# Optimization experiments

Hardware: AMD Instinct MI355X
Metric: run time of the kernel (lower is better)

Reference implementation:

```python
import jax, jax.numpy as jnp
import numpy as np

D_MODEL = 1024
N_HEADS = 16
HEAD_DIM = D_MODEL // N_HEADS


def setup_inputs() -> dict:
    key = jax.random.key(0)
    k1, k2, k3, k4, k5 = jax.random.split(key, 5)
    s = 0.02
    return {
        "x": jax.random.normal(k1, (2, 2048, D_MODEL), dtype=jnp.float32),
        "w_qkv": jax.random.normal(k2, (D_MODEL, 3 * D_MODEL), dtype=jnp.float32) * s,
        "b_qkv": jax.random.normal(k3, (3 * D_MODEL,), dtype=jnp.float32) * s,
        "w_proj": jax.random.normal(k4, (D_MODEL, D_MODEL), dtype=jnp.float32) * s,
        "b_proj": jax.random.normal(k5, (D_MODEL,), dtype=jnp.float32) * s,
    }


def reference(x, w_qkv, b_qkv, w_proj, b_proj):
    B, T, C = x.shape
    # fused qkv projection: [B,T,3C] -> [3,B,H,T,Dh]
    qkv = x @ w_qkv + b_qkv
    qkv = qkv.reshape(B, T, 3, N_HEADS, HEAD_DIM).transpose(2, 0, 3, 1, 4)
    q, k, v = qkv[0], qkv[1], qkv[2]
    scale = 1.0 / np.sqrt(HEAD_DIM).astype(np.float32)
    att = jnp.einsum("bhtd,bhsd->bhts", q, k) * scale  # [B,H,T,T]
    causal = jnp.triu(jnp.ones((T, T), dtype=bool), k=1)
    att = jnp.where(causal, -jnp.inf, att)
    att = jax.nn.softmax(att, axis=-1)
    # dropout is identity in eval / p=0
    out = jnp.einsum("bhts,bhsd->bhtd", att, v)  # [B,H,T,Dh]
    out = out.transpose(0, 2, 1, 3).reshape(B, T, C)
    return out @ w_proj + b_proj
```

## Files before the change

### kernel.cpp

```cpp
#include <hip/hip_runtime.h>
#include <hip/hip_bf16.h>
#include <stdint.h>

#define MROWS 4096
#define DMODEL 1024
#define NQKV 3072
#define TSEQ 2048

typedef __attribute__((ext_vector_type(8))) short short8;
typedef __attribute__((ext_vector_type(4))) short short4v;
typedef __attribute__((ext_vector_type(4))) float floatx4;
typedef unsigned short ushort_t;

#define TILE_ELEMS 4608
#define BH_TILE_STRIDE 147456

#define QSCALE 0.1803368801111204f

static __device__ __forceinline__ unsigned short f2bf(float f) {
    union { float f; unsigned u; } v; v.f = f;
    unsigned r = v.u + 0x7fff + ((v.u >> 16) & 1);
    return (unsigned short)(r >> 16);
}


static __device__ __forceinline__ floatx4 mfma16(short4v a, short4v b, floatx4 c) {
#if defined(__HIP_DEVICE_COMPILE__)
#if __has_builtin(__builtin_amdgcn_mfma_f32_16x16x16bf16_1k)
    return __builtin_amdgcn_mfma_f32_16x16x16bf16_1k(a, b, c, 0, 0, 0);
#else
#error "mfma 16x16x16 bf16 builtin unavailable on device"
#endif
#else
    return c;
#endif
}

static __device__ __forceinline__ unsigned pk2bf(float a, float b) {
    unsigned ua = __float_as_uint(a) + 0x8000u;
    unsigned ub = __float_as_uint(b) + 0x8000u;
#if defined(__HIP_DEVICE_COMPILE__) && __has_builtin(__builtin_amdgcn_perm)
    return __builtin_amdgcn_perm(ub, ua, 0x07060302u);
#else
    return (ua >> 16) | (ub & 0xFFFF0000u);
#endif
}

static __device__ __forceinline__ float exp2_fast(float x) {
#if defined(__HIP_DEVICE_COMPILE__) && __has_builtin(__builtin_amdgcn_exp2f)
    return __builtin_amdgcn_exp2f(x);
#else
    return exp2f(x);
#endif
}

static __device__ __forceinline__ void glds16(const void* g, void* l) {
    __builtin_amdgcn_global_load_lds(
        (const __attribute__((address_space(1))) void*)g,
        (__attribute__((address_space(3))) void*)l, 16, 0, 0);
}

__global__ void cast_f32_bf16(const float* __restrict__ in,
                              ushort_t* __restrict__ out, int n) {
    int i = (blockIdx.x * blockDim.x + threadIdx.x) * 4;
    if (i < n) {
        float4 f = *(const float4*)(in + i);
        ushort4 o;
        o.x = f2bf(f.x); o.y = f2bf(f.y); o.z = f2bf(f.z); o.w = f2bf(f.w);
        *(ushort4*)(out + i) = o;
    }
}

__global__ void transpose_cast(const float* __restrict__ in,
                               ushort_t* __restrict__ out, int R, int C) {
    __shared__ float tile[32][33];
    int c0 = blockIdx.x * 32, r0 = blockIdx.y * 32;
    int tx = threadIdx.x & 31, ty = threadIdx.x >> 5;
    for (int i = 0; i < 4; i++) {
        int r = ty + i * 8;
        tile[r][tx] = in[(size_t)(r0 + r) * C + c0 + tx];
    }
    __syncthreads();
    for (int i = 0; i < 4; i++) {
        int r = ty + i * 8;
        out[(size_t)(c0 + r) * R + r0 + tx] = f2bf(tile[tx][r]);
    }
}

__global__ void transpose_v(const ushort_t* __restrict__ in,
                            ushort_t* __restrict__ out) {
    __shared__ ushort_t T[64][72];
    int tile = blockIdx.x, bh = blockIdx.y;
    int tid = threadIdx.x;
    int row = tid >> 2, q4 = tid & 3;
    const ushort_t* ip = in + ((size_t)bh * TSEQ + tile * 64) * 64;
#pragma unroll
    for (int p = 0; p < 2; p++) {
        int c = q4 * 16 + p * 8;
        *(uint4*)(&T[row][c]) = *(const uint4*)(ip + (size_t)row * 64 + c);
    }
    __syncthreads();
    ushort_t* op = out + (size_t)bh * BH_TILE_STRIDE + (size_t)tile * TILE_ELEMS;
#pragma unroll
    for (int p = 0; p < 2; p++) {
        int cbase = q4 * 16 + p * 8;
        ushort_t tmp[8];
#pragma unroll
        for (int e = 0; e < 8; e++) {
            int cp = cbase + e;
            int Q = cp >> 4, SB = (cp >> 2) & 3, J = cp & 3;
            int s = SB * 16 + Q * 4 + J;
            tmp[e] = T[s][row];
        }
        *(uint4*)(op + (size_t)row * 72 + cbase) = *(uint4*)tmp;
    }
}

template <int EPI, int MFRAG, int PERXCD>
__global__ __launch_bounds__(256, 3)
void gemm_glds(const ushort_t* __restrict__ A,
               const ushort_t* __restrict__ Bt,
               const float* __restrict__ bias,
               void* __restrict__ out0, void* __restrict__ out1, void* __restrict__ out2,
               int M, int N, int K) {
    __shared__ ushort_t As[MFRAG * 32 * 32];
    __shared__ ushort_t Bs[128 * 32];
    int tid = threadIdx.x;
    int wave = tid >> 6, lane = tid & 63;
    int quad = lane >> 4, l16 = lane & 15;
    int id = blockIdx.x;
    int xcd = id & 7, sidx = id >> 3;
    int m_idx = xcd * PERXCD + (sidx & (PERXCD - 1));
    int n_idx = sidx / PERXCD;
    int m0 = m_idx * (MFRAG * 32), n0 = n_idx * 128;
    int wm = (wave & 1) * (MFRAG * 16), wn = (wave >> 1) * 64;

    const floatx4 zero = {0.f, 0.f, 0.f, 0.f};
    floatx4 acc[MFRAG][4];
#pragma unroll
    for (int i = 0; i < MFRAG; i++)
#pragma unroll
        for (int j = 0; j < 4; j++) acc[i][j] = zero;

    int srow = tid >> 2, sc = tid & 3;
    const ushort_t* ag = A  + (size_t)(m0 + srow) * K + sc * 8;
    const ushort_t* bg = Bt + (size_t)(n0 + srow) * K + sc * 8;
    ushort_t* asw = As + wave * 512;
    ushort_t* bsw = Bs + wave * 512;

    for (int k0 = 0; k0 < K; k0 += 32) {
        glds16(ag + k0, asw);
        if (MFRAG == 4) glds16(ag + (size_t)64 * K + k0, asw + 2048);
        glds16(bg + k0, bsw);
        glds16(bg + (size_t)64 * K + k0, bsw + 2048);
        __syncthreads();
        short8 af[MFRAG], bf[4];
#pragma unroll
        for (int i = 0; i < MFRAG; i++)
            af[i] = *(const short8*)(As + (wm + i * 16 + l16) * 32 + quad * 8);
#pragma unroll
        for (int j = 0; j < 4; j++)
            bf[j] = *(const short8*)(Bs + (wn + j * 16 + l16) * 32 + quad * 8);
#pragma unroll
        for (int i = 0; i < MFRAG; i++)
#pragma unroll
            for (int j = 0; j < 4; j++)
                acc[i][j] = __builtin_amdgcn_mfma_f32_16x16x32_bf16(
                    af[i], bf[j], acc[i][j], 0, 0, 0);
        __syncthreads();
    }

    int sec = n0 >> 10;
    ushort_t* dst = (ushort_t*)(sec == 0 ? out0 : (sec == 1 ? out1 : out2));
#pragma unroll
    for (int i = 0; i < MFRAG; i++) {
        int row = m0 + wm + i * 16 + quad * 4;
#pragma unroll
        for (int j = 0; j < 4; j++) {
            int col = n0 + wn + j * 16 + l16;
            float bvs = bias[col];
#pragma unroll
            for (int r = 0; r < 4; r++) {
                float v = acc[i][j][r] + bvs;
                int rowr = row + r;
                if (EPI == 0) {
                    ((float*)out0)[(size_t)rowr * N + col] = v;
                } else {
                    int b = rowr >> 11, t = rowr & 2047;
                    int within = col & 1023, h = within >> 6, d = within & 63;
                    size_t bh = (size_t)(b * 16 + h);
                    if (sec == 0)
                        dst[(bh * 2048 + t) * 64 + d] = f2bf(v * QSCALE);
                    else if (sec == 1)
                        dst[bh * BH_TILE_STRIDE + (size_t)(t >> 6) * TILE_ELEMS
                            + (size_t)(t & 63) * 72 + d] = f2bf(v);
                    else
                        dst[(bh * 2048 + t) * 64 + d] = f2bf(v);
                }
            }
        }
    }
}

__global__ __launch_bounds__(256, 1)
void attn_kernel(const ushort_t* __restrict__ Qb,
                 const ushort_t* __restrict__ Kt,
                 const ushort_t* __restrict__ Vt,
                 ushort_t* __restrict__ outb) {
    __shared__ ushort_t Ks[2][64 * 72];
    __shared__ ushort_t Vs[2][64 * 72];
    int tid = threadIdx.x;
    int wave = tid >> 6, lane = tid & 63;
    int quad = lane >> 4, l16 = lane & 15;
    int pair = blockIdx.x;
    int bh = blockIdx.y;
    int b = bh >> 4, h = bh & 15;
    const ushort_t* qh = Qb + (size_t)bh * TSEQ * 64;
    const ushort_t* kh = Kt + (size_t)bh * BH_TILE_STRIDE;
    const ushort_t* vh = Vt + (size_t)bh * BH_TILE_STRIDE;
    const floatx4 zero = {0.f, 0.f, 0.f, 0.f};
    int lo8 = lane * 8;

    for (int half = 0; half < 2; half++) {
        int qt = half ? (31 - pair) : pair;
        int q0 = qt * 64;
        int nsteps = qt + 1;

        int qrow = q0 + wave * 16 + l16;
        short8 qf0 = *(const short8*)(qh + (size_t)qrow * 64 + quad * 8);
        short8 qf1 = *(const short8*)(qh + (size_t)qrow * 64 + 32 + quad * 8);

        floatx4 Oacc[4];
#pragma unroll
        for (int j = 0; j < 4; j++) Oacc[j] = zero;
        float lsum = 0.f;

#pragma unroll
        for (int c = 0; c < 3; c++) {
            int cc = wave + 4 * c;
            if (cc < 9) {
                glds16(kh + cc * 512 + lo8, &Ks[0][cc * 512]);
                glds16(vh + cc * 512 + lo8, &Vs[0][cc * 512]);
            }
        }

        for (int step = 0; step < nsteps; step++) {
            int cur = step & 1;
            __syncthreads();
            if (step + 1 < nsteps) {
                const ushort_t* kt = kh + (size_t)(step + 1) * TILE_ELEMS;
                const ushort_t* vt = vh + (size_t)(step + 1) * TILE_ELEMS;
#pragma unroll
                for (int c = 0; c < 3; c++) {
                    int cc = wave + 4 * c;
                    if (cc < 9) {
                        glds16(kt + cc * 512 + lo8, &Ks[cur ^ 1][cc * 512]);
                        glds16(vt + cc * 512 + lo8, &Vs[cur ^ 1][cc * 512]);
                    }
                }
            }
            const ushort_t* ks = &Ks[cur][0];
            const ushort_t* vs = &Vs[cur][0];

            floatx4 S[4];
#pragma unroll
            for (int sb = 0; sb < 4; sb++) {
                short8 kf0 = *(const short8*)(ks + (sb * 16 + l16) * 72 + quad * 8);
                short8 kf1 = *(const short8*)(ks + (sb * 16 + l16) * 72 + 32 + quad * 8);
                floatx4 s = zero;
                s = __builtin_amdgcn_mfma_f32_16x16x32_bf16(kf0, qf0, s, 0, 0, 0);
                s = __builtin_amdgcn_mfma_f32_16x16x32_bf16(kf1, qf1, s, 0, 0, 0);
                S[sb] = s;
            }
            if (step == nsteps - 1) {
                int ql = wave * 16 + l16;
#pragma unroll
                for (int sb = 0; sb < 4; sb++)
#pragma unroll
                    for (int r = 0; r < 4; r++)
                        if (sb * 16 + quad * 4 + r > ql) S[sb][r] = -1e30f;
            }
            float sum = 0.f;
#pragma unroll
            for (int sb = 0; sb < 4; sb++)
#pragma unroll
                for (int r = 0; r < 4; r++) {
                    float p = exp2_fast(S[sb][r]);
                    S[sb][r] = p;
                    sum += p;
                }
            lsum += sum;

            short4v pf[4];
#pragma unroll
            for (int sb = 0; sb < 4; sb++) {
                union { unsigned u[2]; short4v v; } pk;
                pk.u[0] = pk2bf(S[sb][0], S[sb][1]);
                pk.u[1] = pk2bf(S[sb][2], S[sb][3]);
                pf[sb] = pk.v;
            }
#pragma unroll
            for (int jd = 0; jd < 4; jd++) {
                const ushort_t* vrow = vs + (jd * 16 + l16) * 72 + quad * 16;
                short8 vA = *(const short8*)(vrow);
                short8 vB = *(const short8*)(vrow + 8);
                short4v v0 = __builtin_shufflevector(vA, vA, 0, 1, 2, 3);
                short4v v1 = __builtin_shufflevector(vA, vA, 4, 5, 6, 7);
                short4v v2 = __builtin_shufflevector(vB, vB, 0, 1, 2, 3);
                short4v v3 = __builtin_shufflevector(vB, vB, 4, 5, 6, 7);
                Oacc[jd] = mfma16(v0, pf[0], Oacc[jd]);
                Oacc[jd] = mfma16(v1, pf[1], Oacc[jd]);
                Oacc[jd] = mfma16(v2, pf[2], Oacc[jd]);
                Oacc[jd] = mfma16(v3, pf[3], Oacc[jd]);
            }
        }
        {
            float l = lsum;
            l += __shfl_xor(l, 16);
            l += __shfl_xor(l, 32);
            float rl = 1.0f / l;
            int row = b * TSEQ + q0 + wave * 16 + l16;
#pragma unroll
            for (int jd = 0; jd < 4; jd++) {
                int col = h * 64 + jd * 16 + quad * 4;
                ushort4 o;
                o.x = f2bf(Oacc[jd][0] * rl);
                o.y = f2bf(Oacc[jd][1] * rl);
                o.z = f2bf(Oacc[jd][2] * rl);
                o.w = f2bf(Oacc[jd][3] * rl);
                *(ushort4*)(outb + (size_t)row * DMODEL + col) = o;
            }
        }
        __syncthreads();
    }
}

extern "C" void kernel_launch(void* const* d_in, const int* in_sizes, int n_in,
                              void* d_out, int out_size, void* d_ws, size_t ws_size,
                              hipStream_t stream) {
    const float* x      = (const float*)d_in[0];
    const float* w_qkv  = (const float*)d_in[1];
    const float* b_qkv  = (const float*)d_in[2];
    const float* w_proj = (const float*)d_in[3];
    const float* b_proj = (const float*)d_in[4];
    float* out = (float*)d_out;
    char* ws = (char*)d_ws;

    ushort_t* xb     = (ushort_t*)(ws);
    ushort_t* Vt     = (ushort_t*)(ws);
    ushort_t* wqkvT  = (ushort_t*)(ws + 8388608);
    ushort_t* wprojT = (ushort_t*)(ws + 10485760);
    ushort_t* Qb     = (ushort_t*)(ws + 14680064);
    ushort_t* Kt     = (ushort_t*)(ws + 23068672);
    ushort_t* Vb     = (ushort_t*)(ws + 32505856);
    ushort_t* attnb  = Vb;

    cast_f32_bf16<<<4096, 256, 0, stream>>>(x, xb, MROWS * DMODEL);
    transpose_cast<<<dim3(NQKV / 32, DMODEL / 32), 256, 0, stream>>>(w_qkv, wqkvT, DMODEL, NQKV);

    gemm_glds<1, 4, 4><<<768, 256, 0, stream>>>(
        xb, wqkvT, b_qkv, Qb, Kt, Vb, MROWS, NQKV, DMODEL);

    transpose_v<<<dim3(32, 32), 256, 0, stream>>>(Vb, Vt);
    transpose_cast<<<dim3(DMODEL / 32, DMODEL / 32), 256, 0, stream>>>(w_proj, wprojT, DMODEL, DMODEL);

    attn_kernel<<<dim3(16, 32), 256, 0, stream>>>(Qb, Kt, Vt, attnb);

    gemm_glds<0, 2, 8><<<512, 256, 0, stream>>>(
        attnb, wprojT, b_proj, out, nullptr, nullptr, MROWS, DMODEL, DMODEL);
}
```

Baseline: 197.0 us.

## Split attention into one block per query tile with longest-first scheduling

The attention kernel no longer pairs two query tiles per block. It launches 1024 independent blocks ordered longest-first and spread across heads, and raises launch bounds to allow four blocks per CU, aiming for better occupancy and load balance under the causal mask. It also computes the softmax row sum with an MFMA against a ones vector instead of scalar adds and shuffles, uses the hardware packed bf16 convert instruction, and adds s_setprio around the MFMA sections. These changes risk more scheduling overhead and register pressure, and the ones-MFMA sum uses bf16-rounded probabilities.

Result: no change. 195.4 us (-0.8%).

```diff
diff --git a/kernel.cpp b/kernel.cpp
--- a/kernel.cpp
+++ b/kernel.cpp
@@ -43,6 +43,16 @@
     return __builtin_amdgcn_perm(ub, ua, 0x07060302u);
 #else
     return (ua >> 16) | (ub & 0xFFFF0000u);
+#endif
+}
+
+static __device__ __forceinline__ unsigned cvtpk(float a, float b) {
+#if defined(__HIP_DEVICE_COMPILE__)
+    unsigned r;
+    asm("v_cvt_pk_bf16_f32 %0, %1, %2" : "=v"(r) : "v"(a), "v"(b));
+    return r;
+#else
+    return pk2bf(a, b);
 #endif
 }
 
@@ -202,7 +212,7 @@
     }
 }
 
-__global__ __launch_bounds__(256, 1)
+__global__ __launch_bounds__(256, 4)
 void attn_kernel(const ushort_t* __restrict__ Qb,
                  const ushort_t* __restrict__ Kt,
                  const ushort_t* __restrict__ Vt,
@@ -212,126 +222,125 @@
     int tid = threadIdx.x;
     int wave = tid >> 6, lane = tid & 63;
     int quad = lane >> 4, l16 = lane & 15;
-    int pair = blockIdx.x;
-    int bh = blockIdx.y;
+    int id = blockIdx.x;
+    int g = id >> 3;
+    int bh = (id & 7) * 4 + (g >> 5);
+    int qt = 31 - (g & 31);
     int b = bh >> 4, h = bh & 15;
     const ushort_t* qh = Qb + (size_t)bh * TSEQ * 64;
     const ushort_t* kh = Kt + (size_t)bh * BH_TILE_STRIDE;
     const ushort_t* vh = Vt + (size_t)bh * BH_TILE_STRIDE;
     const floatx4 zero = {0.f, 0.f, 0.f, 0.f};
+    const short4v ones = {(short)0x3F80, (short)0x3F80, (short)0x3F80, (short)0x3F80};
     int lo8 = lane * 8;
 
-    for (int half = 0; half < 2; half++) {
-        int qt = half ? (31 - pair) : pair;
-        int q0 = qt * 64;
-        int nsteps = qt + 1;
-
-        int qrow = q0 + wave * 16 + l16;
-        short8 qf0 = *(const short8*)(qh + (size_t)qrow * 64 + quad * 8);
-        short8 qf1 = *(const short8*)(qh + (size_t)qrow * 64 + 32 + quad * 8);
-
-        floatx4 Oacc[4];
-#pragma unroll
-        for (int j = 0; j < 4; j++) Oacc[j] = zero;
-        float lsum = 0.f;
-
-#pragma unroll
-        for (int c = 0; c < 3; c++) {
-            int cc = wave + 4 * c;
-            if (cc < 9) {
-                glds16(kh + cc * 512 + lo8, &Ks[0][cc * 512]);
-                glds16(vh + cc * 512 + lo8, &Vs[0][cc * 512]);
-            }
-        }
-
-        for (int step = 0; step < nsteps; step++) {
-            int cur = step & 1;
-            __syncthreads();
-            if (step + 1 < nsteps) {
-                const ushort_t* kt = kh + (size_t)(step + 1) * TILE_ELEMS;
-                const ushort_t* vt = vh + (size_t)(step + 1) * TILE_ELEMS;
-#pragma unroll
-                for (int c = 0; c < 3; c++) {
-                    int cc = wave + 4 * c;
-                    if (cc < 9) {
-                        glds16(kt + cc * 512 + lo8, &Ks[cur ^ 1][cc * 512]);
-                        glds16(vt + cc * 512 + lo8, &Vs[cur ^ 1][cc * 512]);
-                    }
+    int q0 = qt * 64;
+    int nsteps = qt + 1;
+
+    int qrow = q0 + wave * 16 + l16;
+    short8 qf0 = *(const short8*)(qh + (size_t)qrow * 64 + quad * 8);
+    short8 qf1 = *(const short8*)(qh + (size_t)qrow * 64 + 32 + quad * 8);
+
+    floatx4 Oacc[4];
+#pragma unroll
+    for (int j = 0; j < 4; j++) Oacc[j] = zero;
+    floatx4 lacc = zero;
+
+#pragma unroll
+    for (int c = 0; c < 3; c++) {
+        int cc = wave + 4 * c;
+        if (cc < 9) {
+            glds16(kh + cc * 512 + lo8, &Ks[0][cc * 512]);
+            glds16(vh + cc * 512 + lo8, &Vs[0][cc * 512]);
+        }
+    }
+
+    for (int step = 0; step < nsteps; step++) {
+        int cur = step & 1;
+        __syncthreads();
+        if (step + 1 < nsteps) {
+            const ushort_t* kt = kh + (size_t)(step + 1) * TILE_ELEMS;
+            const ushort_t* vt = vh + (size_t)(step + 1) * TILE_ELEMS;
+#pragma unroll
+            for (int c = 0; c < 3; c++) {
+                int cc = wave + 4 * c;
+                if (cc < 9) {
+                    glds16(kt + cc * 512 + lo8, &Ks[cur ^ 1][cc * 512]);
+                    glds16(vt + cc * 512 + lo8, &Vs[cur ^ 1][cc * 512]);
                 }
             }
-            const ushort_t* ks = &Ks[cur][0];
-            const ushort_t* vs = &Vs[cur][0];
-
-            floatx4 S[4];
-#pragma unroll
-            for (int sb = 0; sb < 4; sb++) {
-                short8 kf0 = *(const short8*)(ks + (sb * 16 + l16) * 72 + quad * 8);
-                short8 kf1 = *(const short8*)(ks + (sb * 16 + l16) * 72 + 32 + quad * 8);
-                floatx4 s = zero;
-                s = __builtin_amdgcn_mfma_f32_16x16x32_bf16(kf0, qf0, s, 0, 0, 0);
-                s = __builtin_amdgcn_mfma_f32_16x16x32_bf16(kf1, qf1, s, 0, 0, 0);
-                S[sb] = s;
-            }
-            if (step == nsteps - 1) {
-                int ql = wave * 16 + l16;
-#pragma unroll
-                for (int sb = 0; sb < 4; sb++)
-#pragma unroll
-                    for (int r = 0; r < 4; r++)
-                        if (sb * 16 + quad * 4 + r > ql) S[sb][r] = -1e30f;
-            }
-            float sum = 0.f;
+        }
+        const ushort_t* ks = &Ks[cur][0];
+        const ushort_t* vs = &Vs[cur][0];
+
+        floatx4 S[4];
+        __builtin_amdgcn_s_setprio(1);
+#pragma unroll
+        for (int sb = 0; sb < 4; sb++) {
+            short8 kf0 = *(const short8*)(ks + (sb * 16 + l16) * 72 + quad * 8);
+            short8 kf1 = *(const short8*)(ks + (sb * 16 + l16) * 72 + 32 + quad * 8);
+            floatx4 s = zero;
+            s = __builtin_amdgcn_mfma_f32_16x16x32_bf16(kf0, qf0, s, 0, 0, 0);
+            s = __builtin_amdgcn_mfma_f32_16x16x32_bf16(kf1, qf1, s, 0, 0, 0);
+            S[sb] = s;
+        }
+        __builtin_amdgcn_s_setprio(0);
+        if (step == nsteps - 1) {
+            int ql = wave * 16 + l16;
 #pragma unroll
             for (int sb = 0; sb < 4; sb++)
 #pragma unroll
-                for (int r = 0; r < 4; r++) {
-                    float p = exp2_fast(S[sb][r]);
-                    S[sb][r] = p;
-                    sum += p;
-                }
-            lsum += sum;
-
-            short4v pf[4];
-#pragma unroll
-            for (int sb = 0; sb < 4; sb++) {
-                union { unsigned u[2]; short4v v; } pk;
-                pk.u[0] = pk2bf(S[sb][0], S[sb][1]);
-                pk.u[1] = pk2bf(S[sb][2], S[sb][3]);
-                pf[sb] = pk.v;
-            }
-#pragma unroll
-            for (int jd = 0; jd < 4; jd++) {
-                const ushort_t* vrow = vs + (jd * 16 + l16) * 72 + quad * 16;
-                short8 vA = *(const short8*)(vrow);
-                short8 vB = *(const short8*)(vrow + 8);
-                short4v v0 = __builtin_shufflevector(vA, vA, 0, 1, 2, 3);
-                short4v v1 = __builtin_shufflevector(vA, vA, 4, 5, 6, 7);
-                short4v v2 = __builtin_shufflevector(vB, vB, 0, 1, 2, 3);
-                short4v v3 = __builtin_shufflevector(vB, vB, 4, 5, 6, 7);
-                Oacc[jd] = mfma16(v0, pf[0], Oacc[jd]);
-                Oacc[jd] = mfma16(v1, pf[1], Oacc[jd]);
-                Oacc[jd] = mfma16(v2, pf[2], Oacc[jd]);
-                Oacc[jd] = mfma16(v3, pf[3], Oacc[jd]);
-            }
-        }
-        {
-            float l = lsum;
-            l += __shfl_xor(l, 16);
-            l += __shfl_xor(l, 32);
-            float rl = 1.0f / l;
-            int row = b * TSEQ + q0 + wave * 16 + l16;
-#pragma unroll
-            for (int jd = 0; jd < 4; jd++) {
-                int col = h * 64 + jd * 16 + quad * 4;
-                ushort4 o;
-                o.x = f2bf(Oacc[jd][0] * rl);
-                o.y = f2bf(Oacc[jd][1] * rl);
-                o.z = f2bf(Oacc[jd][2] * rl);
-                o.w = f2bf(Oacc[jd][3] * rl);
-                *(ushort4*)(outb + (size_t)row * DMODEL + col) = o;
-            }
-        }
-        __syncthreads();
+                for (int r = 0; r < 4; r++)
+                    if (sb * 16 + quad * 4 + r > ql) S[sb][r] = -1e30f;
+        }
+#pragma unroll
+        for (int sb = 0; sb < 4; sb++)
+#pragma unroll
+            for (int r = 0; r < 4; r++)
+                S[sb][r] = exp2_fast(S[sb][r]);
+
+        short4v pf[4];
+#pragma unroll
+        for (int sb = 0; sb < 4; sb++) {
+            union { unsigned u[2]; short4v v; } pk;
+            pk.u[0] = cvtpk(S[sb][0], S[sb][1]);
+            pk.u[1] = cvtpk(S[sb][2], S[sb][3]);
+            pf[sb] = pk.v;
+        }
+        __builtin_amdgcn_s_setprio(1);
+        lacc = mfma16(ones, pf[0], lacc);
+        lacc = mfma16(ones, pf[1], lacc);
+        lacc = mfma16(ones, pf[2], lacc);
+        lacc = mfma16(ones, pf[3], lacc);
+#pragma unroll
+        for (int jd = 0; jd < 4; jd++) {
+            const ushort_t* vrow = vs + (jd * 16 + l16) * 72 + quad * 16;
+            short8 vA = *(const short8*)(vrow);
+            short8 vB = *(const short8*)(vrow + 8);
+            short4v v0 = __builtin_shufflevector(vA, vA, 0, 1, 2, 3);
+            short4v v1 = __builtin_shufflevector(vA, vA, 4, 5, 6, 7);
+            short4v v2 = __builtin_shufflevector(vB, vB, 0, 1, 2, 3);
+            short4v v3 = __builtin_shufflevector(vB, vB, 4, 5, 6, 7);
+            Oacc[jd] = mfma16(v0, pf[0], Oacc[jd]);
+            Oacc[jd] = mfma16(v1, pf[1], Oacc[jd]);
+            Oacc[jd] = mfma16(v2, pf[2], Oacc[jd]);
+            Oacc[jd] = mfma16(v3, pf[3], Oacc[jd]);
+        }
+        __builtin_amdgcn_s_setprio(0);
+    }
+    {
+        float rl = 1.0f / lacc[0];
+        int row = b * TSEQ + q0 + wave * 16 + l16;
+#pragma unroll
+        for (int jd = 0; jd < 4; jd++) {
+            int col = h * 64 + jd * 16 + quad * 4;
+            ushort4 o;
+            o.x = f2bf(Oacc[jd][0] * rl);
+            o.y = f2bf(Oacc[jd][1] * rl);
+            o.z = f2bf(Oacc[jd][2] * rl);
+            o.w = f2bf(Oacc[jd][3] * rl);
+            *(ushort4*)(outb + (size_t)row * DMODEL + col) = o;
+        }
     }
 }
 
@@ -364,7 +373,7 @@
     transpose_v<<<dim3(32, 32), 256, 0, stream>>>(Vb, Vt);
     transpose_cast<<<dim3(DMODEL / 32, DMODEL / 32), 256, 0, stream>>>(w_proj, wprojT, DMODEL, DMODEL);
 
-    attn_kernel<<<dim3(16, 32), 256, 0, stream>>>(Qb, Kt, Vt, attnb);
+    attn_kernel<<<dim3(1024), 256, 0, stream>>>(Qb, Kt, Vt, attnb);
 
     gemm_glds<0, 2, 8><<<512, 256, 0, stream>>>(
         attnb, wprojT, b_proj, out, nullptr, nullptr, MROWS, DMODEL, DMODEL);
```
